# Performance work log

Measured on AMD Instinct MI355X. Metric: run time of the kernel, lower is better.

## Reference

```python
import jax, jax.numpy as jnp
import numpy as np
from jax import lax

K = 20        # cfgs.k: knn size for edge-conv graph features
OUT_K = 8     # cfgs.out_k: knn size for output aggregation
OUT_DIM = 256
EPS = 1e-5    # BatchNorm eps (torch default), training-mode batch stats


def _bn(y, g, b, axes):
    m = y.mean(axes, keepdims=True)
    v = y.var(axes, keepdims=True)  # biased var, as torch BN uses for normalization
    return (y - m) * lax.rsqrt(v + EPS) * g + b


def _graph_feature(x, k):
    # x: [B,N,C] -> [B,N,k,2C] = concat(neighbor - center, center)
    xx = jnp.sum(x * x, axis=-1)                          # [B,N]
    inner = jnp.einsum('bnc,bmc->bnm', x, x)              # [B,N,N]
    neg_d = 2.0 * inner - xx[:, :, None] - xx[:, None, :]  # -||xi-xj||^2
    idx = lax.top_k(neg_d, k)[1]                          # [B,N,k] nearest (incl. self)
    nbr = jax.vmap(lambda p, i: p[i])(x, idx)             # [B,N,k,C]
    ctr = jnp.broadcast_to(x[:, :, None, :], nbr.shape)
    return jnp.concatenate([nbr - ctr, ctr], axis=-1)


def _edgeconv(x, w, g, b):
    # x: [B,N,C] -> [B,N,O]; conv2d 1x1 (no bias) + BN + LeakyReLU(0.2) + max over k
    f = _graph_feature(x, K)                              # [B,N,K,2C]
    y = jnp.einsum('bnkc,oc->bnko', f, w)
    y = jax.nn.leaky_relu(_bn(y, g, b, (0, 1, 2)), 0.2)
    return y.max(axis=2)


def _fps(pts, npoint):
    # furthest point sampling, start at index 0 (pointnet2 convention). pts: [B,N,3]
    B, N, _ = pts.shape
    d0 = jnp.full((B, N), 1e10, pts.dtype)
    first = jnp.zeros((B,), jnp.int32)

    def step(carry, _):
        dist, last = carry
        lp = jnp.take_along_axis(pts, last[:, None, None], axis=1)  # [B,1,3]
        d = jnp.sum((pts - lp) ** 2, axis=-1)
        dist = jnp.minimum(dist, d)
        nxt = jnp.argmax(dist, axis=-1).astype(jnp.int32)
        return (dist, nxt), nxt

    _, rest = lax.scan(step, (d0, first), None, length=npoint - 1)
    return jnp.concatenate([first[:, None], rest.T], axis=1)  # [B,npoint]


def reference(x, w1, g1, b1, w2, g2, b2, wf, gf, bf, wc, gc, bc):
    B, N, _ = x.shape
    # edge-conv block 1: 6 -> 64
    x1 = _edgeconv(x, w1, g1, b1)                         # [B,N,64]
    n1 = N // 2
    _ = _fps(x, n1)  # points[1]; unused when f_layer == c_layer == 2
    # edge-conv block 2: 128 -> 64
    x2 = _edgeconv(x1, w2, g2, b2)                        # [B,N,64]
    n2 = n1 // 2
    idx2 = _fps(x, n2)                                    # [B,M]
    p2 = jax.vmap(lambda p, i: p[i])(x, idx2)             # [B,M,3]
    # KNN(support=x points, query=p2): indices of OUT_K nearest support points
    d = jnp.sum((p2[:, :, None, :] - x[:, None, :, :]) ** 2, axis=-1)  # [B,M,N]
    knn_idx = lax.top_k(-d, OUT_K)[1]                     # [B,M,OUT_K]
    # gather neighbor features from x2 and mean over neighbors
    agg = jax.vmap(lambda f, i: f[i])(x2, knn_idx).mean(axis=2)        # [B,M,64]
    f_out = _bn(jnp.einsum('bmc,oc->bmo', agg, wf), gf, bf, (0, 1)).transpose(0, 2, 1)
    c_out = _bn(jnp.einsum('bmc,oc->bmo', agg, wc), gc, bc, (0, 1)).transpose(0, 2, 1)
    mask = jnp.ones((B, n2), dtype=bool)
    return (f_out, c_out, p2, p2, mask, mask)


def setup_inputs() -> dict:
    key = jax.random.key(0)
    ks = jax.random.split(key, 6)
    B, N = 4, 4096
    x = jax.random.normal(ks[0], (B, N, 3), jnp.float32)
    def w(k, o, c):
        return jax.random.normal(k, (o, c), jnp.float32) / np.sqrt(c)
    return {
        'x': x,
        'w1': w(ks[1], 64, 6),   'g1': jnp.ones(64),  'b1': jnp.zeros(64),
        'w2': w(ks[2], 64, 128), 'g2': jnp.ones(64),  'b2': jnp.zeros(64),
        'wf': w(ks[3], OUT_DIM, 64), 'gf': jnp.ones(OUT_DIM), 'bf': jnp.zeros(OUT_DIM),
        'wc': w(ks[4], OUT_DIM, 64), 'gc': jnp.ones(OUT_DIM), 'bc': jnp.zeros(OUT_DIM),
    }
```

## Files before the change

### kernel.cpp

```cpp
#include <hip/hip_runtime.h>

#define WB 4
#define WN 4096
#define WKNN 20
#define WM 1024
#define WOUTK 8
#define WOD 256
#define BEPS 1e-5f

typedef unsigned long long u64;
typedef unsigned int u32;

#define ACC_F    0
#define IDX1_I   2048
#define IDX2NN_I 329728
#define IDX2_I   657408
#define X1_F     661504
#define XX1_F    1710080
#define X2_F     1726464

#define O_F   0
#define O_C   1048576
#define O_P2A 2097152
#define O_P2B 2109440
#define O_M0  2121728
#define O_M1  2125824

__device__ __forceinline__ u64 shflx64(u64 v, int m){
    int lo = __shfl_xor((int)(u32)(v & 0xFFFFFFFFull), m, 64);
    int hi = __shfl_xor((int)(u32)(v >> 32), m, 64);
    return ((u64)(u32)hi << 32) | (u32)lo;
}
__device__ __forceinline__ u32 encf(float d){
    u32 u = __float_as_uint(d);
    return (u & 0x80000000u) ? ~u : (u | 0x80000000u);
}
template<int L>
__device__ __forceinline__ void ins(u64* lst, u64 key){
    if (key < lst[L-1]){
        #pragma unroll
        for (int j = 0; j < L; ++j){
            u64 a = lst[j];
            u64 mn = key < a ? key : a;
            u64 mx = key < a ? a : key;
            lst[j] = mn; key = mx;
        }
    }
}

template<int CTRL, int RM>
__device__ __forceinline__ void dppsel(double& k, float& x, float& y, float& z){
    int lo = __double2loint(k), hi = __double2hiint(k);
    int slo = __builtin_amdgcn_update_dpp(lo, lo, CTRL, RM, 0xF, false);
    int shi = __builtin_amdgcn_update_dpp(hi, hi, CTRL, RM, 0xF, false);
    int sx = __builtin_amdgcn_update_dpp(__float_as_int(x), __float_as_int(x), CTRL, RM, 0xF, false);
    int sy = __builtin_amdgcn_update_dpp(__float_as_int(y), __float_as_int(y), CTRL, RM, 0xF, false);
    int sz = __builtin_amdgcn_update_dpp(__float_as_int(z), __float_as_int(z), CTRL, RM, 0xF, false);
    double ok = __hiloint2double(shi, slo);
    bool t = ok > k;
    k = t ? ok : k;
    x = t ? __int_as_float(sx) : x;
    y = t ? __int_as_float(sy) : y;
    z = t ? __int_as_float(sz) : z;
}

__global__ __launch_bounds__(512,1)
void k1_fps_knn1(const float* __restrict__ x, float* __restrict__ out,
                 int* __restrict__ idx1, int* __restrict__ idx2){
    __shared__ float px[WN], py[WN], pz[WN];
    __shared__ double wk[2][4];
    __shared__ float wx4[2][4], wy4[2][4], wz4[2][4];
    int tid = threadIdx.x;
    if (blockIdx.x < 4){
        int b = (int)blockIdx.x;
        const float* xb = x + b*WN*3;
        if (tid >= 256){
            for (int i = tid-256; i < WM; i += 256){
                out[O_M0 + b*WM + i] = 1.0f;
                out[O_M1 + b*WM + i] = 1.0f;
            }
            for (int it=1; it<WM; ++it) __syncthreads();
        } else {
            float ptx[16],pty[16],ptz[16],dst[16];
            #pragma unroll
            for (int j=0;j<16;++j){
                int p = tid + j*256;
                ptx[j]=xb[p*3]; pty[j]=xb[p*3+1]; ptz[j]=xb[p*3+2];
                dst[j]=1e10f;
            }
            float lx=xb[0], ly=xb[1], lz=xb[2];
            if (tid==0){
                idx2[b*WM] = 0;
                int o3 = (b*WM)*3;
                out[O_P2A+o3]=lx; out[O_P2A+o3+1]=ly; out[O_P2A+o3+2]=lz;
                out[O_P2B+o3]=lx; out[O_P2B+o3+1]=ly; out[O_P2B+o3+2]=lz;
            }
            int w = tid>>6, lane = tid&63;
            for (int it=1; it<WM; ++it){
                double bk = -1.0; float bx=lx, by=ly, bz=lz;
                #pragma unroll
                for (int j=0;j<16;++j){
                    float dx=ptx[j]-lx, dy=pty[j]-ly, dz=ptz[j]-lz;
                    float d = dx*dx + dy*dy + dz*dz;
                    d = fminf(dst[j], d); dst[j] = d;
                    double kd = __hiloint2double(__float_as_int(d),
                                                 4095 - (tid + j*256));
                    bool t = kd > bk;
                    bk = t?kd:bk; bx = t?ptx[j]:bx; by = t?pty[j]:by; bz = t?ptz[j]:bz;
                }
                dppsel<0x111,0xF>(bk,bx,by,bz);
                dppsel<0x112,0xF>(bk,bx,by,bz);
                dppsel<0x114,0xF>(bk,bx,by,bz);
                dppsel<0x118,0xF>(bk,bx,by,bz);
                dppsel<0x142,0xA>(bk,bx,by,bz);
                dppsel<0x143,0xC>(bk,bx,by,bz);
                int ib = it & 1;
                if (lane==63){ wk[ib][w]=bk; wx4[ib][w]=bx; wy4[ib][w]=by; wz4[ib][w]=bz; }
                __syncthreads();
                int e = lane & 3;
                double gk = wk[ib][e];
                float gx = wx4[ib][e], gy = wy4[ib][e], gz = wz4[ib][e];
                dppsel<0xB1,0xF>(gk,gx,gy,gz);
                dppsel<0x4E,0xF>(gk,gx,gy,gz);
                lx = gx; ly = gy; lz = gz;
                if (tid==0){
                    int last = 4095 - (int)(u32)__double2loint(gk);
                    idx2[b*WM+it] = last;
                    int o3 = (b*WM+it)*3;
                    out[O_P2A+o3]=lx; out[O_P2A+o3+1]=ly; out[O_P2A+o3+2]=lz;
                    out[O_P2B+o3]=lx; out[O_P2B+o3+1]=ly; out[O_P2B+o3+2]=lz;
                }
            }
        }
    } else {
        int kb = (int)blockIdx.x - 4;
        int b = kb >> 9;
        const float* xb = x + b*WN*3;
        for (int i = tid; i < WN*3; i += 512){
            float v = xb[i];
            int n = i/3, c = i - n*3;
            if (c==0) px[n]=v; else if (c==1) py[n]=v; else pz[n]=v;
        }
        __syncthreads();
        int wid = tid>>6, lane = tid&63;
        int n = (kb & 511)*8 + wid;
        int grow = b*WN + n;
        float qx=px[n], qy=py[n], qz=pz[n];
        float qq = qx*qx+qy*qy+qz*qz;
        u64 lst[WKNN];
        #pragma unroll
        for (int j=0;j<WKNN;++j) lst[j]=~0ull;
        for (int t=0;t<64;++t){
            int c = lane + t*64;
            float sx=px[c], sy=py[c], sz=pz[c];
            float ss = sx*sx+sy*sy+sz*sz;
            float inner = qx*sx+qy*sy+qz*sz;
            float nd = (2.0f*inner - qq) - ss;
            u64 key = ((u64)(0xFFFFFFFFu - encf(nd))<<32) | (u32)c;
            ins<WKNN>(lst, key);
        }
        int ob = grow*WKNN;
        for (int r=0;r<WKNN;++r){
            u64 k = lst[0];
            #pragma unroll
            for (int m=32;m;m>>=1){ u64 o = shflx64(k,m); k = o<k?o:k; }
            if (lane==0) idx1[ob+r] = (int)(k & 0xFFFFFFFFu);
            if (lst[0]==k){
                #pragma unroll
                for (int j=0;j<WKNN-1;++j) lst[j]=lst[j+1];
                lst[WKNN-1]=~0ull;
            }
        }
    }
}

__global__ __launch_bounds__(256,1)
void k2_ec1_stats(const float* __restrict__ x, const float* __restrict__ w1,
                  const int* __restrict__ idx1, float* __restrict__ acc){
    __shared__ float as[64], aq[64];
    int tid = threadIdx.x;
    if (tid < 64){ as[tid]=0.f; aq[tid]=0.f; }
    __syncthreads();
    int cg = tid & 7, sg = tid >> 3;
    int chb = cg*8;
    float w[8][6];
    #pragma unroll
    for (int i=0;i<8;++i){
        #pragma unroll
        for (int j=0;j<6;++j) w[i][j] = w1[(chb+i)*6+j];
    }
    float s[8]={0,0,0,0,0,0,0,0}, q[8]={0,0,0,0,0,0,0,0};
    int s0 = (int)blockIdx.x*1024 + sg*32;
    for (int i=0;i<32;++i){
        int smp = s0+i;
        int bn = smp/WKNN;
        int j = idx1[smp];
        int bb = bn >> 12;
        const float* ct = x + bn*3;
        const float* nb = x + (bb*WN + j)*3;
        float c0=ct[0],c1=ct[1],c2=ct[2];
        float f0=nb[0]-c0, f1=nb[1]-c1, f2=nb[2]-c2;
        #pragma unroll
        for (int c=0;c<8;++c){
            float y = w[c][0]*f0 + w[c][1]*f1 + w[c][2]*f2
                    + w[c][3]*c0 + w[c][4]*c1 + w[c][5]*c2;
            s[c] += y; q[c] = fmaf(y,y,q[c]);
        }
    }
    #pragma unroll
    for (int c=0;c<8;++c){ atomicAdd(&as[chb+c], s[c]); atomicAdd(&aq[chb+c], q[c]); }
    __syncthreads();
    if (tid < 64){ atomicAdd(&acc[tid], as[tid]); atomicAdd(&acc[64+tid], aq[tid]); }
}

__global__ __launch_bounds__(256,1)
void k4_ec1_apply(const float* __restrict__ x, const float* __restrict__ w1,
                  const float* __restrict__ g1, const float* __restrict__ b1,
                  const int* __restrict__ idx1, const float* __restrict__ acc,
                  float* __restrict__ x1){
    int lin = (int)blockIdx.x*256 + threadIdx.x;
    int row = lin >> 3, cg = lin & 7, chb = cg*8;
    int bb = row >> 12;
    const float Pinv = 1.0f/(float)(WB*WN*WKNN);
    float aa[8], cc[8], w[8][6];
    #pragma unroll
    for (int i=0;i<8;++i){
        int ch = chb+i;
        float mean = acc[ch]*Pinv;
        float var  = acc[64+ch]*Pinv - mean*mean;
        float rstd = rsqrtf(var + BEPS);
        aa[i] = g1[ch]*rstd;
        cc[i] = b1[ch] - mean*aa[i];
        #pragma unroll
        for (int j=0;j<6;++j) w[i][j]=w1[ch*6+j];
    }
    const float* ct = x + row*3;
    float c0=ct[0],c1=ct[1],c2=ct[2];
    float mx[8];
    #pragma unroll
    for (int i=0;i<8;++i) mx[i] = -1e30f;
    for (int k=0;k<WKNN;++k){
        int j = idx1[row*WKNN+k];
        const float* nb = x + (bb*WN + j)*3;
        float f0=nb[0]-c0, f1=nb[1]-c1, f2=nb[2]-c2;
        #pragma unroll
        for (int c=0;c<8;++c){
            float y = w[c][0]*f0 + w[c][1]*f1 + w[c][2]*f2
                    + w[c][3]*c0 + w[c][4]*c1 + w[c][5]*c2;
            float v = fmaf(y, aa[c], cc[c]);
            v = fmaxf(v, 0.2f*v);
            mx[c] = fmaxf(mx[c], v);
        }
    }
    #pragma unroll
    for (int c=0;c<8;++c) x1[row*64 + chb + c] = mx[c];
}

__global__ __launch_bounds__(256,1)
void k5_xx1(const float* __restrict__ x1, float* __restrict__ xx1){
    int wid = threadIdx.x>>6, lane = threadIdx.x&63;
    int row = (int)blockIdx.x*4 + wid;
    float v = x1[row*64+lane];
    float s = v*v;
    #pragma unroll
    for (int m=32;m;m>>=1) s += __shfl_xor(s,m,64);
    if (lane==0) xx1[row]=s;
}

__global__ __launch_bounds__(512,1)
void k6_knn2(const float* __restrict__ x1, const float* __restrict__ xx1,
             int* __restrict__ idx2nn){
    __shared__ __align__(16) float Qt[64*64];
    __shared__ __align__(16) float St[128*68];
    __shared__ float Sxx[128];
    float* Dt = St;
    int tid = threadIdx.x, wid = tid>>6, lane = tid&63;
    int b = (int)blockIdx.x >> 6, qt = (int)blockIdx.x & 63;
    const float* xb = x1 + b*WN*64;
    for (int i=tid; i<64*16; i+=512){
        int r = i>>4, c4 = i&15;
        *(float4*)&Qt[r*64 + c4*4] = *(const float4*)&xb[(qt*64+r)*64 + c4*4];
    }
    float qxx[8];
    #pragma unroll
    for (int i=0;i<8;++i) qxx[i] = xx1[b*WN + qt*64 + wid*8 + i];
    u64 lst[WKNN];
    #pragma unroll
    for (int j=0;j<WKNN;++j) lst[j]=~0ull;
    int sq = tid>>3, seg = tid&7;
    for (int ct=0; ct<32; ++ct){
        int cb = ct*128;
        __syncthreads();
        for (int i=tid; i<128*16; i+=512){
            int r=i>>4, c4=i&15;
            *(float4*)&St[r*68 + c4*4] = *(const float4*)&xb[(cb+r)*64 + c4*4];
        }
        if (tid < 128) Sxx[tid] = xx1[b*WN + cb + tid];
        __syncthreads();
        float acc[8][2];
        #pragma unroll
        for (int i=0;i<8;++i){ acc[i][0]=0.f; acc[i][1]=0.f; }
        #pragma unroll 4
        for (int d4=0; d4<16; ++d4){
            float4 s0 = *(const float4*)&St[lane*68 + d4*4];
            float4 s1 = *(const float4*)&St[(lane+64)*68 + d4*4];
            #pragma unroll
            for (int i=0;i<8;++i){
                float4 qv = *(const float4*)&Qt[(wid*8+i)*64 + d4*4];
                acc[i][0] += qv.x*s0.x + qv.y*s0.y + qv.z*s0.z + qv.w*s0.w;
                acc[i][1] += qv.x*s1.x + qv.y*s1.y + qv.z*s1.z + qv.w*s1.w;
            }
        }
        __syncthreads();
        float sx0 = Sxx[lane], sx1 = Sxx[lane+64];
        #pragma unroll
        for (int i=0;i<8;++i){
            int r = wid*8+i;
            Dt[r*132 + lane]      = (2.0f*acc[i][0] - qxx[i]) - sx0;
            Dt[r*132 + lane + 64] = (2.0f*acc[i][1] - qxx[i]) - sx1;
        }
        __syncthreads();
        #pragma unroll
        for (int m=0;m<16;++m){
            int col = seg*16+m;
            float nd = Dt[sq*132 + col];
            u64 key = ((u64)(0xFFFFFFFFu - encf(nd))<<32) | (u32)(cb+col);
            ins<WKNN>(lst,key);
        }
    }
    int ob = (b*WN + qt*64 + sq)*WKNN;
    for (int r=0;r<WKNN;++r){
        u64 k = lst[0];
        #pragma unroll
        for (int m=4;m;m>>=1){ u64 o=shflx64(k,m); k = o<k?o:k; }
        if ((tid&7)==0) idx2nn[ob+r] = (int)(k & 0xFFFFFFFFu);
        if (lst[0]==k){
            #pragma unroll
            for (int j=0;j<WKNN-1;++j) lst[j]=lst[j+1];
            lst[WKNN-1]=~0ull;
        }
    }
}

__global__ __launch_bounds__(512,1)
void k7_ec2_stats(const float* __restrict__ x1, const float* __restrict__ w2,
                  const int* __restrict__ idx2nn, float* __restrict__ acc){
    __shared__ __align__(16) float wsm[64*128];
    __shared__ float as[64], aq[64];
    int tid = threadIdx.x, wid = tid>>6, lane = tid&63;
    for (int i=tid; i<2048; i+=512)
        *(float4*)&wsm[i*4] = *(const float4*)&w2[i*4];
    if (tid<64){ as[tid]=0.f; aq[tid]=0.f; }
    __syncthreads();
    int row = (int)blockIdx.x*64 + lane;
    int b = row >> 12;
    const float* xr  = x1 + row*64;
    const float* xbb = x1 + b*WN*64;
    float ss[8]={0,0,0,0,0,0,0,0}, qs[8]={0,0,0,0,0,0,0,0};
    for (int kc=0; kc<5; ++kc){
        int jj[4];
        #pragma unroll
        for (int kk=0;kk<4;++kk) jj[kk] = idx2nn[row*WKNN + kc*4 + kk];
        float av[8][4];
        #pragma unroll
        for (int c=0;c<8;++c){ av[c][0]=0;av[c][1]=0;av[c][2]=0;av[c][3]=0; }
        #pragma unroll 4
        for (int dc=0; dc<16; ++dc){
            float4 cv = *(const float4*)&xr[dc*4];
            float4 fv[4];
            #pragma unroll
            for (int kk=0;kk<4;++kk){
                float4 nv = *(const float4*)&xbb[jj[kk]*64 + dc*4];
                fv[kk].x=nv.x-cv.x; fv[kk].y=nv.y-cv.y; fv[kk].z=nv.z-cv.z; fv[kk].w=nv.w-cv.w;
            }
            #pragma unroll
            for (int c=0;c<8;++c){
                float4 wv = *(const float4*)&wsm[(wid*8+c)*128 + dc*4];
                #pragma unroll
                for (int kk=0;kk<4;++kk)
                    av[c][kk] += wv.x*fv[kk].x + wv.y*fv[kk].y + wv.z*fv[kk].z + wv.w*fv[kk].w;
            }
        }
        #pragma unroll 4
        for (int dc=16; dc<32; ++dc){
            float4 cv = *(const float4*)&xr[(dc-16)*4];
            #pragma unroll
            for (int c=0;c<8;++c){
                float4 wv = *(const float4*)&wsm[(wid*8+c)*128 + dc*4];
                float dv = wv.x*cv.x + wv.y*cv.y + wv.z*cv.z + wv.w*cv.w;
                #pragma unroll
                for (int kk=0;kk<4;++kk) av[c][kk] += dv;
            }
        }
        #pragma unroll
        for (int c=0;c<8;++c){
            #pragma unroll
            for (int kk=0;kk<4;++kk){ ss[c]+=av[c][kk]; qs[c]=fmaf(av[c][kk],av[c][kk],qs[c]); }
        }
    }
    #pragma unroll
    for (int c=0;c<8;++c){ atomicAdd(&as[wid*8+c], ss[c]); atomicAdd(&aq[wid*8+c], qs[c]); }
    __syncthreads();
    if (tid<64){ atomicAdd(&acc[128+tid], as[tid]); atomicAdd(&acc[192+tid], aq[tid]); }
}

__global__ __launch_bounds__(512,1)
void k9_ec2_apply(const float* __restrict__ x1, const float* __restrict__ w2,
                  const float* __restrict__ g2, const float* __restrict__ b2,
                  const int* __restrict__ idx2nn, const float* __restrict__ acc,
                  float* __restrict__ x2){
    __shared__ __align__(16) float wsm[64*128];
    int tid = threadIdx.x, wid = tid>>6, lane = tid&63;
    for (int i=tid; i<2048; i+=512)
        *(float4*)&wsm[i*4] = *(const float4*)&w2[i*4];
    __syncthreads();
    const float Pinv = 1.0f/(float)(WB*WN*WKNN);
    float aa[8], cc[8];
    #pragma unroll
    for (int c=0;c<8;++c){
        int ch = wid*8+c;
        float mean = acc[128+ch]*Pinv;
        float var  = acc[192+ch]*Pinv - mean*mean;
        float rstd = rsqrtf(var + BEPS);
        aa[c] = g2[ch]*rstd;
        cc[c] = b2[ch] - mean*aa[c];
    }
    int row = (int)blockIdx.x*64 + lane;
    int b = row>>12;
    const float* xr  = x1 + row*64;
    const float* xbb = x1 + b*WN*64;
    float mx[8];
    #pragma unroll
    for (int c=0;c<8;++c) mx[c] = -1e30f;
    for (int kc=0;kc<5;++kc){
        int jj[4];
        #pragma unroll
        for (int kk=0;kk<4;++kk) jj[kk]=idx2nn[row*WKNN+kc*4+kk];
        float av[8][4];
        #pragma unroll
        for (int c=0;c<8;++c){ av[c][0]=0;av[c][1]=0;av[c][2]=0;av[c][3]=0; }
        #pragma unroll 4
        for (int dc=0;dc<16;++dc){
            float4 cv = *(const float4*)&xr[dc*4];
            float4 fv[4];
            #pragma unroll
            for (int kk=0;kk<4;++kk){
                float4 nv = *(const float4*)&xbb[jj[kk]*64 + dc*4];
                fv[kk].x=nv.x-cv.x; fv[kk].y=nv.y-cv.y; fv[kk].z=nv.z-cv.z; fv[kk].w=nv.w-cv.w;
            }
            #pragma unroll
            for (int c=0;c<8;++c){
                float4 wv = *(const float4*)&wsm[(wid*8+c)*128 + dc*4];
                #pragma unroll
                for (int kk=0;kk<4;++kk)
                    av[c][kk] += wv.x*fv[kk].x + wv.y*fv[kk].y + wv.z*fv[kk].z + wv.w*fv[kk].w;
            }
        }
        #pragma unroll 4
        for (int dc=16;dc<32;++dc){
            float4 cv = *(const float4*)&xr[(dc-16)*4];
            #pragma unroll
            for (int c=0;c<8;++c){
                float4 wv = *(const float4*)&wsm[(wid*8+c)*128 + dc*4];
                float dv = wv.x*cv.x + wv.y*cv.y + wv.z*cv.z + wv.w*cv.w;
                #pragma unroll
                for (int kk=0;kk<4;++kk) av[c][kk] += dv;
            }
        }
        #pragma unroll
        for (int c=0;c<8;++c){
            #pragma unroll
            for (int kk=0;kk<4;++kk){
                float v = fmaf(av[c][kk], aa[c], cc[c]);
                v = fmaxf(v, 0.2f*v);
                mx[c] = fmaxf(mx[c], v);
            }
        }
    }
    #pragma unroll
    for (int c=0;c<8;++c) x2[row*64 + wid*8 + c] = mx[c];
}

__global__ __launch_bounds__(256,1)
void k10_out(const float* __restrict__ x, const float* __restrict__ x2,
             const int* __restrict__ idx2, const float* __restrict__ wf,
             const float* __restrict__ wc, float* __restrict__ out,
             float* __restrict__ acc){
    __shared__ float px[WN], py[WN], pz[WN];
    __shared__ __align__(16) float aggs[4][64];
    __shared__ float sacc[1024];
    int tid=threadIdx.x, wid=tid>>6, lane=tid&63;
    int b = (int)blockIdx.x >> 6;
    int mb = ((int)blockIdx.x & 63)*16;
    const float* xb = x + b*WN*3;
    for (int i=tid;i<WN*3;i+=256){
        float v=xb[i]; int n=i/3,c=i-n*3;
        if(c==0)px[n]=v; else if(c==1)py[n]=v; else pz[n]=v;
    }
    for (int i=tid;i<1024;i+=256) sacc[i]=0.f;
    __syncthreads();
    for (int qq=0;qq<4;++qq){
        int m = mb + wid*4 + qq;
        int pi = idx2[b*WM+m];
        float qx=px[pi], qy=py[pi], qz=pz[pi];
        u64 lst[WOUTK];
        #pragma unroll
        for (int j=0;j<WOUTK;++j) lst[j]=~0ull;
        for (int t=0;t<64;++t){
            int c = lane + t*64;
            float dx=qx-px[c], dy=qy-py[c], dz=qz-pz[c];
            float d = dx*dx+dy*dy+dz*dz;
            u64 key = ((u64)encf(d)<<32) | (u32)c;
            ins<WOUTK>(lst,key);
        }
        int jr[WOUTK];
        #pragma unroll
        for (int r=0;r<WOUTK;++r){
            u64 k=lst[0];
            #pragma unroll
            for (int mm=32;mm;mm>>=1){ u64 o=shflx64(k,mm); k = o<k?o:k; }
            jr[r] = (int)(k&0xFFFFFFFFu);
            if (lst[0]==k){
                #pragma unroll
                for (int j=0;j<WOUTK-1;++j) lst[j]=lst[j+1];
                lst[WOUTK-1]=~0ull;
            }
        }
        float a = 0.f;
        #pragma unroll
        for (int r=0;r<WOUTK;++r) a += x2[(b*WN + jr[r])*64 + lane];
        a *= 0.125f;
        aggs[wid][lane] = a;
        __syncthreads();
        #pragma unroll
        for (int i=0;i<4;++i){
            int o = lane + 64*i;
            const float4* wfp = (const float4*)(wf + o*64);
            const float4* wcp = (const float4*)(wc + o*64);
            float af=0.f, ac=0.f;
            #pragma unroll
            for (int d4=0;d4<16;++d4){
                float4 avv = *(const float4*)&aggs[wid][d4*4];
                float4 w1v = wfp[d4];
                float4 w2v = wcp[d4];
                af += w1v.x*avv.x + w1v.y*avv.y + w1v.z*avv.z + w1v.w*avv.w;
                ac += w2v.x*avv.x + w2v.y*avv.y + w2v.z*avv.z + w2v.w*avv.w;
            }
            out[O_F + (b*WOD + o)*WM + m] = af;
            out[O_C + (b*WOD + o)*WM + m] = ac;
            atomicAdd(&sacc[o],       af);
            atomicAdd(&sacc[256+o],   af*af);
            atomicAdd(&sacc[512+o],   ac);
            atomicAdd(&sacc[768+o],   ac*ac);
        }
        __syncthreads();
    }
    for (int i=tid;i<1024;i+=256) atomicAdd(&acc[256+i], sacc[i]);
}

__global__ __launch_bounds__(256,1)
void k12_final(const float* __restrict__ acc,
               const float* __restrict__ gf, const float* __restrict__ bf,
               const float* __restrict__ gc, const float* __restrict__ bc,
               float* __restrict__ out){
    int t = (int)blockIdx.x*256 + threadIdx.x;
    int half = t >> 20;
    int r = t & 0xFFFFF;
    int o = (r >> 10) & 255;
    const float Pinv = 1.0f/4096.0f;
    float sum = acc[(half?768:256) + o];
    float sq  = acc[(half?1024:512) + o];
    float mean = sum*Pinv;
    float var  = sq*Pinv - mean*mean;
    float rstd = rsqrtf(var + BEPS);
    float g  = half ? gc[o] : gf[o];
    float bb = half ? bc[o] : bf[o];
    float y = out[t];
    out[t] = (y-mean)*rstd*g + bb;
}

extern "C" void kernel_launch(void* const* d_in, const int* in_sizes, int n_in,
                              void* d_out, int out_size, void* d_ws, size_t ws_size,
                              hipStream_t stream){
    const float* x  = (const float*)d_in[0];
    const float* w1 = (const float*)d_in[1];
    const float* g1 = (const float*)d_in[2];
    const float* b1 = (const float*)d_in[3];
    const float* w2 = (const float*)d_in[4];
    const float* g2 = (const float*)d_in[5];
    const float* b2 = (const float*)d_in[6];
    const float* wf = (const float*)d_in[7];
    const float* gf = (const float*)d_in[8];
    const float* bf = (const float*)d_in[9];
    const float* wc = (const float*)d_in[10];
    const float* gc = (const float*)d_in[11];
    const float* bc = (const float*)d_in[12];
    float* out = (float*)d_out;
    float* wsf = (float*)d_ws;
    int*   wsi = (int*)d_ws;
    float* ACC    = wsf + ACC_F;
    int*   idx1   = wsi + IDX1_I;
    int*   idx2nn = wsi + IDX2NN_I;
    int*   idx2   = wsi + IDX2_I;
    float* x1     = wsf + X1_F;
    float* xx1    = wsf + XX1_F;
    float* x2     = wsf + X2_F;

    hipMemsetAsync(ACC, 0, 1280*sizeof(float), stream);
    k1_fps_knn1 <<<2052,512,0,stream>>>(x,out,idx1,idx2);
    k2_ec1_stats<<<320, 256, 0,stream>>>(x,w1,idx1,ACC);
    k4_ec1_apply<<<512, 256, 0,stream>>>(x,w1,g1,b1,idx1,ACC,x1);
    k5_xx1      <<<4096,256, 0,stream>>>(x1,xx1);
    k6_knn2     <<<256, 512, 0,stream>>>(x1,xx1,idx2nn);
    k7_ec2_stats<<<256, 512, 0,stream>>>(x1,w2,idx2nn,ACC);
    k9_ec2_apply<<<256, 512, 0,stream>>>(x1,w2,g2,b2,idx2nn,ACC,x2);
    k10_out     <<<256, 256, 0,stream>>>(x,x2,idx2,wf,wc,out,ACC);
    k12_final   <<<8192,256, 0,stream>>>(ACC,gf,bf,gc,bc,out);
}
```

Measured before the change: 2.004 ms.

## Fuse all stages into one persistent kernel with software grid barriers

Replaces the chain of nine kernel launches with a single persistent kernel. Four blocks run FPS concurrently while 256 worker blocks step through knn1, the edge-conv stats and apply, knn2, the output stage and the final BN, separated by atomic-counter grid barriers. The FPS blocks now use all 512 threads with 8 points each and an 8-wave reduction, and FPS is overlapped with the rest of the pipeline through a flag. This removes launch gaps and lets the serial FPS hide behind other work, at the cost of relying on all 260 blocks being co-resident and on spin barriers that have timeout escapes.

```diff
diff --git a/kernel.cpp b/kernel.cpp
--- a/kernel.cpp
+++ b/kernel.cpp
@@ -12,6 +12,8 @@
 typedef unsigned int u32;
 
 #define ACC_F    0
+#define CTR_WBAR 1280
+#define CTR_FPS  1281
 #define IDX1_I   2048
 #define IDX2NN_I 329728
 #define IDX2_I   657408
@@ -64,107 +66,314 @@
     z = t ? __int_as_float(sz) : z;
 }
 
+struct SmemA { float px[WN], py[WN], pz[WN]; double wk[2][8]; float wx[2][8], wy[2][8], wz[2][8]; };
+struct SmemB { float Qt[64*64]; float St[128*68]; float Sxx[128]; };
+struct SmemC { float wsm[64*128]; float as[64], aq[64]; };
+struct SmemD { float px[WN], py[WN], pz[WN]; float aggs[8][64]; float sacc[1024]; };
+union Smem { SmemA a; SmemB b; SmemC c; SmemD d; };
+
+__device__ __forceinline__ void wbar(u32* ctr, u32 target){
+    __syncthreads();
+    if (threadIdx.x == 0){
+        __threadfence();
+        __hip_atomic_fetch_add(ctr, 1u, __ATOMIC_ACQ_REL, __HIP_MEMORY_SCOPE_AGENT);
+        long long spins = 0;
+        while (__hip_atomic_load(ctr, __ATOMIC_ACQUIRE, __HIP_MEMORY_SCOPE_AGENT) < target){
+            __builtin_amdgcn_s_sleep(8);
+            if (++spins > (1LL<<22)) break;
+        }
+        __threadfence();
+    }
+    __syncthreads();
+}
+__device__ __forceinline__ void wait_flag(u32* ctr, u32 target){
+    __syncthreads();
+    if (threadIdx.x == 0){
+        long long spins = 0;
+        while (__hip_atomic_load(ctr, __ATOMIC_ACQUIRE, __HIP_MEMORY_SCOPE_AGENT) < target){
+            __builtin_amdgcn_s_sleep(8);
+            if (++spins > (1LL<<22)) break;
+        }
+        __threadfence();
+    }
+    __syncthreads();
+}
+
 __global__ __launch_bounds__(512,1)
-void k1_fps_knn1(const float* __restrict__ x, float* __restrict__ out,
-                 int* __restrict__ idx1, int* __restrict__ idx2){
-    __shared__ float px[WN], py[WN], pz[WN];
-    __shared__ double wk[2][4];
-    __shared__ float wx4[2][4], wy4[2][4], wz4[2][4];
+void mega(const float* __restrict__ x,
+          const float* __restrict__ w1, const float* __restrict__ g1, const float* __restrict__ b1,
+          const float* __restrict__ w2, const float* __restrict__ g2, const float* __restrict__ b2,
+          const float* __restrict__ wf, const float* __restrict__ gf, const float* __restrict__ bf,
+          const float* __restrict__ wc, const float* __restrict__ gc, const float* __restrict__ bc,
+          float* __restrict__ out, float* __restrict__ wsf, int* __restrict__ wsi)
+{
+    __shared__ Smem sm;
+    float* acc    = wsf + ACC_F;
+    int*   idx1   = wsi + IDX1_I;
+    int*   idx2nn = wsi + IDX2NN_I;
+    int*   idx2   = wsi + IDX2_I;
+    float* x1     = wsf + X1_F;
+    float* xx1    = wsf + XX1_F;
+    float* x2     = wsf + X2_F;
+    u32* wctr = (u32*)(wsi + CTR_WBAR);
+    u32* fctr = (u32*)(wsi + CTR_FPS);
     int tid = threadIdx.x;
+
     if (blockIdx.x < 4){
         int b = (int)blockIdx.x;
         const float* xb = x + b*WN*3;
-        if (tid >= 256){
-            for (int i = tid-256; i < WM; i += 256){
-                out[O_M0 + b*WM + i] = 1.0f;
-                out[O_M1 + b*WM + i] = 1.0f;
-            }
-            for (int it=1; it<WM; ++it) __syncthreads();
-        } else {
-            float ptx[16],pty[16],ptz[16],dst[16];
-            #pragma unroll
-            for (int j=0;j<16;++j){
-                int p = tid + j*256;
-                ptx[j]=xb[p*3]; pty[j]=xb[p*3+1]; ptz[j]=xb[p*3+2];
-                dst[j]=1e10f;
-            }
-            float lx=xb[0], ly=xb[1], lz=xb[2];
+        for (int i = tid; i < WM; i += 512){
+            out[O_M0 + b*WM + i] = 1.0f;
+            out[O_M1 + b*WM + i] = 1.0f;
+        }
+        float ptx[8],pty[8],ptz[8],dst[8];
+        #pragma unroll
+        for (int j=0;j<8;++j){
+            int p = tid + j*512;
+            ptx[j]=xb[p*3]; pty[j]=xb[p*3+1]; ptz[j]=xb[p*3+2];
+            dst[j]=1e10f;
+        }
+        float lx=xb[0], ly=xb[1], lz=xb[2];
+        if (tid==0){
+            idx2[b*WM] = 0;
+            int o3 = (b*WM)*3;
+            out[O_P2A+o3]=lx; out[O_P2A+o3+1]=ly; out[O_P2A+o3+2]=lz;
+            out[O_P2B+o3]=lx; out[O_P2B+o3+1]=ly; out[O_P2B+o3+2]=lz;
+        }
+        int w = tid>>6, lane = tid&63;
+        int base = 4095 - tid;
+        for (int it=1; it<WM; ++it){
+            double bk = -1.0; float bx=lx, by=ly, bz=lz;
+            #pragma unroll
+            for (int j=0;j<8;++j){
+                float dx=ptx[j]-lx, dy=pty[j]-ly, dz=ptz[j]-lz;
+                float d = dx*dx + dy*dy + dz*dz;
+                d = fminf(dst[j], d); dst[j] = d;
+                double kd = __hiloint2double(__float_as_int(d), base - j*512);
+                bool t = kd > bk;
+                bk = t?kd:bk; bx = t?ptx[j]:bx; by = t?pty[j]:by; bz = t?ptz[j]:bz;
+            }
+            dppsel<0x111,0xF>(bk,bx,by,bz);
+            dppsel<0x112,0xF>(bk,bx,by,bz);
+            dppsel<0x114,0xF>(bk,bx,by,bz);
+            dppsel<0x118,0xF>(bk,bx,by,bz);
+            dppsel<0x142,0xA>(bk,bx,by,bz);
+            dppsel<0x143,0xC>(bk,bx,by,bz);
+            int ib = it & 1;
+            if (lane==63){ sm.a.wk[ib][w]=bk; sm.a.wx[ib][w]=bx; sm.a.wy[ib][w]=by; sm.a.wz[ib][w]=bz; }
+            __syncthreads();
+            int e = lane & 3;
+            double k0 = sm.a.wk[ib][e],   k1 = sm.a.wk[ib][e+4];
+            float x0 = sm.a.wx[ib][e],   y0 = sm.a.wy[ib][e],   z0 = sm.a.wz[ib][e];
+            float x1v= sm.a.wx[ib][e+4], y1v= sm.a.wy[ib][e+4], z1v= sm.a.wz[ib][e+4];
+            bool t8 = k1 > k0;
+            double gk = t8?k1:k0;
+            float gx = t8?x1v:x0, gy = t8?y1v:y0, gz = t8?z1v:z0;
+            dppsel<0xB1,0xF>(gk,gx,gy,gz);
+            dppsel<0x4E,0xF>(gk,gx,gy,gz);
+            lx = gx; ly = gy; lz = gz;
             if (tid==0){
-                idx2[b*WM] = 0;
-                int o3 = (b*WM)*3;
+                int last = 4095 - (int)(u32)__double2loint(gk);
+                idx2[b*WM+it] = last;
+                int o3 = (b*WM+it)*3;
                 out[O_P2A+o3]=lx; out[O_P2A+o3+1]=ly; out[O_P2A+o3+2]=lz;
                 out[O_P2B+o3]=lx; out[O_P2B+o3+1]=ly; out[O_P2B+o3+2]=lz;
             }
-            int w = tid>>6, lane = tid&63;
-            for (int it=1; it<WM; ++it){
-                double bk = -1.0; float bx=lx, by=ly, bz=lz;
-                #pragma unroll
-                for (int j=0;j<16;++j){
-                    float dx=ptx[j]-lx, dy=pty[j]-ly, dz=ptz[j]-lz;
-                    float d = dx*dx + dy*dy + dz*dz;
-                    d = fminf(dst[j], d); dst[j] = d;
-                    double kd = __hiloint2double(__float_as_int(d),
-                                                 4095 - (tid + j*256));
-                    bool t = kd > bk;
-                    bk = t?kd:bk; bx = t?ptx[j]:bx; by = t?pty[j]:by; bz = t?ptz[j]:bz;
-                }
-                dppsel<0x111,0xF>(bk,bx,by,bz);
-                dppsel<0x112,0xF>(bk,bx,by,bz);
-                dppsel<0x114,0xF>(bk,bx,by,bz);
-                dppsel<0x118,0xF>(bk,bx,by,bz);
-                dppsel<0x142,0xA>(bk,bx,by,bz);
-                dppsel<0x143,0xC>(bk,bx,by,bz);
-                int ib = it & 1;
-                if (lane==63){ wk[ib][w]=bk; wx4[ib][w]=bx; wy4[ib][w]=by; wz4[ib][w]=bz; }
-                __syncthreads();
-                int e = lane & 3;
-                double gk = wk[ib][e];
-                float gx = wx4[ib][e], gy = wy4[ib][e], gz = wz4[ib][e];
-                dppsel<0xB1,0xF>(gk,gx,gy,gz);
-                dppsel<0x4E,0xF>(gk,gx,gy,gz);
-                lx = gx; ly = gy; lz = gz;
-                if (tid==0){
-                    int last = 4095 - (int)(u32)__double2loint(gk);
-                    idx2[b*WM+it] = last;
-                    int o3 = (b*WM+it)*3;
-                    out[O_P2A+o3]=lx; out[O_P2A+o3+1]=ly; out[O_P2A+o3+2]=lz;
-                    out[O_P2B+o3]=lx; out[O_P2B+o3+1]=ly; out[O_P2B+o3+2]=lz;
-                }
-            }
-        }
-    } else {
-        int kb = (int)blockIdx.x - 4;
-        int b = kb >> 9;
-        const float* xb = x + b*WN*3;
+        }
+        __syncthreads();
+        if (tid==0){
+            __threadfence();
+            __hip_atomic_fetch_add(fctr, 1u, __ATOMIC_RELEASE, __HIP_MEMORY_SCOPE_AGENT);
+        }
+        return;
+    }
+
+    int wb = (int)blockIdx.x - 4;
+    int wid = tid>>6, lane = tid&63;
+
+    {
+        int bb = wb >> 6;
+        const float* xbk = x + bb*WN*3;
         for (int i = tid; i < WN*3; i += 512){
-            float v = xb[i];
+            float v = xbk[i];
             int n = i/3, c = i - n*3;
-            if (c==0) px[n]=v; else if (c==1) py[n]=v; else pz[n]=v;
-        }
-        __syncthreads();
-        int wid = tid>>6, lane = tid&63;
-        int n = (kb & 511)*8 + wid;
-        int grow = b*WN + n;
-        float qx=px[n], qy=py[n], qz=pz[n];
-        float qq = qx*qx+qy*qy+qz*qz;
+            if (c==0) sm.a.px[n]=v; else if (c==1) sm.a.py[n]=v; else sm.a.pz[n]=v;
+        }
+        __syncthreads();
+        for (int rr=0; rr<8; ++rr){
+            int n = (wb&63)*64 + wid*8 + rr;
+            float qx=sm.a.px[n], qy=sm.a.py[n], qz=sm.a.pz[n];
+            float qq = qx*qx+qy*qy+qz*qz;
+            u64 lst[WKNN];
+            #pragma unroll
+            for (int j=0;j<WKNN;++j) lst[j]=~0ull;
+            for (int t=0;t<64;++t){
+                int c = lane + t*64;
+                float sx=sm.a.px[c], sy=sm.a.py[c], sz=sm.a.pz[c];
+                float ss = sx*sx+sy*sy+sz*sz;
+                float inner = qx*sx+qy*sy+qz*sz;
+                float nd = (2.0f*inner - qq) - ss;
+                u64 key = ((u64)(0xFFFFFFFFu - encf(nd))<<32) | (u32)c;
+                ins<WKNN>(lst, key);
+            }
+            int ob = (bb*WN + n)*WKNN;
+            for (int r=0;r<WKNN;++r){
+                u64 k = lst[0];
+                #pragma unroll
+                for (int m=32;m;m>>=1){ u64 o = shflx64(k,m); k = o<k?o:k; }
+                if (lane==0) idx1[ob+r] = (int)(k & 0xFFFFFFFFu);
+                if (lst[0]==k){
+                    #pragma unroll
+                    for (int j=0;j<WKNN-1;++j) lst[j]=lst[j+1];
+                    lst[WKNN-1]=~0ull;
+                }
+            }
+        }
+    }
+    wbar(wctr, 256*1);
+
+    {
+        if (tid < 64){ sm.c.as[tid]=0.f; sm.c.aq[tid]=0.f; }
+        __syncthreads();
+        int cg = tid & 7, sg = tid >> 3, chb = cg*8;
+        float w[8][6];
+        #pragma unroll
+        for (int i=0;i<8;++i){
+            #pragma unroll
+            for (int j=0;j<6;++j) w[i][j] = w1[(chb+i)*6+j];
+        }
+        float s[8]={0,0,0,0,0,0,0,0}, q[8]={0,0,0,0,0,0,0,0};
+        int s0 = wb*1280 + sg*20;
+        for (int i=0;i<20;++i){
+            int smp = s0+i;
+            int bn = smp/WKNN;
+            int j = idx1[smp];
+            int bb2 = bn >> 12;
+            const float* ct = x + bn*3;
+            const float* nb = x + (bb2*WN + j)*3;
+            float c0=ct[0],c1=ct[1],c2=ct[2];
+            float f0=nb[0]-c0, f1=nb[1]-c1, f2=nb[2]-c2;
+            #pragma unroll
+            for (int c=0;c<8;++c){
+                float y = w[c][0]*f0 + w[c][1]*f1 + w[c][2]*f2
+                        + w[c][3]*c0 + w[c][4]*c1 + w[c][5]*c2;
+                s[c] += y; q[c] = fmaf(y,y,q[c]);
+            }
+        }
+        #pragma unroll
+        for (int c=0;c<8;++c){ atomicAdd(&sm.c.as[chb+c], s[c]); atomicAdd(&sm.c.aq[chb+c], q[c]); }
+        __syncthreads();
+        if (tid < 64){ atomicAdd(&acc[tid], sm.c.as[tid]); atomicAdd(&acc[64+tid], sm.c.aq[tid]); }
+    }
+    wbar(wctr, 256*2);
+
+    {
+        int lin = wb*512 + tid;
+        int row = lin >> 3, cg = lin & 7, chb = cg*8;
+        int bb2 = row >> 12;
+        const float Pinv = 1.0f/(float)(WB*WN*WKNN);
+        float aa[8], cc[8], w[8][6];
+        #pragma unroll
+        for (int i=0;i<8;++i){
+            int ch = chb+i;
+            float mean = acc[ch]*Pinv;
+            float var  = acc[64+ch]*Pinv - mean*mean;
+            float rstd = rsqrtf(var + BEPS);
+            aa[i] = g1[ch]*rstd;
+            cc[i] = b1[ch] - mean*aa[i];
+            #pragma unroll
+            for (int j=0;j<6;++j) w[i][j]=w1[ch*6+j];
+        }
+        const float* ct = x + row*3;
+        float c0=ct[0],c1=ct[1],c2=ct[2];
+        float mx[8];
+        #pragma unroll
+        for (int i=0;i<8;++i) mx[i] = -1e30f;
+        for (int k=0;k<WKNN;++k){
+            int j = idx1[row*WKNN+k];
+            const float* nb = x + (bb2*WN + j)*3;
+            float f0=nb[0]-c0, f1=nb[1]-c1, f2=nb[2]-c2;
+            #pragma unroll
+            for (int c=0;c<8;++c){
+                float y = w[c][0]*f0 + w[c][1]*f1 + w[c][2]*f2
+                        + w[c][3]*c0 + w[c][4]*c1 + w[c][5]*c2;
+                float v = fmaf(y, aa[c], cc[c]);
+                v = fmaxf(v, 0.2f*v);
+                mx[c] = fmaxf(mx[c], v);
+            }
+        }
+        float sq2 = 0.f;
+        #pragma unroll
+        for (int c=0;c<8;++c){ x1[row*64 + chb + c] = mx[c]; sq2 = fmaf(mx[c],mx[c],sq2); }
+        sq2 += __shfl_xor(sq2,1,64);
+        sq2 += __shfl_xor(sq2,2,64);
+        sq2 += __shfl_xor(sq2,4,64);
+        if ((tid&7)==0) xx1[row] = sq2;
+    }
+    wbar(wctr, 256*3);
+
+    {
+        float* Qt = sm.b.Qt; float* St = sm.b.St; float* Sxx = sm.b.Sxx;
+        float* Dt = St;
+        int b2 = wb >> 6, qt = wb & 63;
+        const float* xbf = x1 + b2*WN*64;
+        for (int i=tid; i<64*16; i+=512){
+            int r = i>>4, c4 = i&15;
+            *(float4*)&Qt[r*64 + c4*4] = *(const float4*)&xbf[(qt*64+r)*64 + c4*4];
+        }
+        float qxx[8];
+        #pragma unroll
+        for (int i=0;i<8;++i) qxx[i] = xx1[b2*WN + qt*64 + wid*8 + i];
         u64 lst[WKNN];
         #pragma unroll
         for (int j=0;j<WKNN;++j) lst[j]=~0ull;
-        for (int t=0;t<64;++t){
-            int c = lane + t*64;
-            float sx=px[c], sy=py[c], sz=pz[c];
-            float ss = sx*sx+sy*sy+sz*sz;
-            float inner = qx*sx+qy*sy+qz*sz;
-            float nd = (2.0f*inner - qq) - ss;
-            u64 key = ((u64)(0xFFFFFFFFu - encf(nd))<<32) | (u32)c;
-            ins<WKNN>(lst, key);
-        }
-        int ob = grow*WKNN;
+        int sq = tid>>3, seg = tid&7;
+        for (int ct=0; ct<32; ++ct){
+            int cb = ct*128;
+            __syncthreads();
+            for (int i=tid; i<128*16; i+=512){
+                int r=i>>4, c4=i&15;
+                *(float4*)&St[r*68 + c4*4] = *(const float4*)&xbf[(cb+r)*64 + c4*4];
+            }
+            if (tid < 128) Sxx[tid] = xx1[b2*WN + cb + tid];
+            __syncthreads();
+            float a2[8][2];
+            #pragma unroll
+            for (int i=0;i<8;++i){ a2[i][0]=0.f; a2[i][1]=0.f; }
+            #pragma unroll 4
+            for (int d4=0; d4<16; ++d4){
+                float4 s0 = *(const float4*)&St[lane*68 + d4*4];
+                float4 s1 = *(const float4*)&St[(lane+64)*68 + d4*4];
+                #pragma unroll
+                for (int i=0;i<8;++i){
+                    float4 qv = *(const float4*)&Qt[(wid*8+i)*64 + d4*4];
+                    a2[i][0] += qv.x*s0.x + qv.y*s0.y + qv.z*s0.z + qv.w*s0.w;
+                    a2[i][1] += qv.x*s1.x + qv.y*s1.y + qv.z*s1.z + qv.w*s1.w;
+                }
+            }
+            __syncthreads();
+            float sx0 = Sxx[lane], sx1 = Sxx[lane+64];
+            #pragma unroll
+            for (int i=0;i<8;++i){
+                int r = wid*8+i;
+                Dt[r*132 + lane]      = (2.0f*a2[i][0] - qxx[i]) - sx0;
+                Dt[r*132 + lane + 64] = (2.0f*a2[i][1] - qxx[i]) - sx1;
+            }
+            __syncthreads();
+            #pragma unroll
+            for (int m=0;m<16;++m){
+                int col = seg*16+m;
+                float nd = Dt[sq*132 + col];
+                u64 key = ((u64)(0xFFFFFFFFu - encf(nd))<<32) | (u32)(cb+col);
+                ins<WKNN>(lst,key);
+            }
+        }
+        int ob = (b2*WN + qt*64 + sq)*WKNN;
         for (int r=0;r<WKNN;++r){
             u64 k = lst[0];
             #pragma unroll
-            for (int m=32;m;m>>=1){ u64 o = shflx64(k,m); k = o<k?o:k; }
-            if (lane==0) idx1[ob+r] = (int)(k & 0xFFFFFFFFu);
+            for (int m=4;m;m>>=1){ u64 o=shflx64(k,m); k = o<k?o:k; }
+            if ((tid&7)==0) idx2nn[ob+r] = (int)(k & 0xFFFFFFFFu);
             if (lst[0]==k){
                 #pragma unroll
                 for (int j=0;j<WKNN-1;++j) lst[j]=lst[j+1];
@@ -172,411 +381,230 @@
             }
         }
     }
-}
-
-__global__ __launch_bounds__(256,1)
-void k2_ec1_stats(const float* __restrict__ x, const float* __restrict__ w1,
-                  const int* __restrict__ idx1, float* __restrict__ acc){
-    __shared__ float as[64], aq[64];
-    int tid = threadIdx.x;
-    if (tid < 64){ as[tid]=0.f; aq[tid]=0.f; }
-    __syncthreads();
-    int cg = tid & 7, sg = tid >> 3;
-    int chb = cg*8;
-    float w[8][6];
-    #pragma unroll
-    for (int i=0;i<8;++i){
-        #pragma unroll
-        for (int j=0;j<6;++j) w[i][j] = w1[(chb+i)*6+j];
-    }
-    float s[8]={0,0,0,0,0,0,0,0}, q[8]={0,0,0,0,0,0,0,0};
-    int s0 = (int)blockIdx.x*1024 + sg*32;
-    for (int i=0;i<32;++i){
-        int smp = s0+i;
-        int bn = smp/WKNN;
-        int j = idx1[smp];
-        int bb = bn >> 12;
-        const float* ct = x + bn*3;
-        const float* nb = x + (bb*WN + j)*3;
-        float c0=ct[0],c1=ct[1],c2=ct[2];
-        float f0=nb[0]-c0, f1=nb[1]-c1, f2=nb[2]-c2;
+    wbar(wctr, 256*4);
+
+    {
+        float* wsm = sm.c.wsm;
+        for (int i=tid; i<2048; i+=512)
+            *(float4*)&wsm[i*4] = *(const float4*)&w2[i*4];
+        if (tid<64){ sm.c.as[tid]=0.f; sm.c.aq[tid]=0.f; }
+        __syncthreads();
+        int row = wb*64 + lane;
+        int b2 = row >> 12;
+        const float* xr  = x1 + row*64;
+        const float* xbb = x1 + b2*WN*64;
+        float ss[8]={0,0,0,0,0,0,0,0}, qs[8]={0,0,0,0,0,0,0,0};
+        for (int kc=0; kc<5; ++kc){
+            int jj[4];
+            #pragma unroll
+            for (int kk=0;kk<4;++kk) jj[kk] = idx2nn[row*WKNN + kc*4 + kk];
+            float av[8][4];
+            #pragma unroll
+            for (int c=0;c<8;++c){ av[c][0]=0;av[c][1]=0;av[c][2]=0;av[c][3]=0; }
+            #pragma unroll 4
+            for (int dc=0; dc<16; ++dc){
+                float4 cv = *(const float4*)&xr[dc*4];
+                float4 fv[4];
+                #pragma unroll
+                for (int kk=0;kk<4;++kk){
+                    float4 nv = *(const float4*)&xbb[jj[kk]*64 + dc*4];
+                    fv[kk].x=nv.x-cv.x; fv[kk].y=nv.y-cv.y; fv[kk].z=nv.z-cv.z; fv[kk].w=nv.w-cv.w;
+                }
+                #pragma unroll
+                for (int c=0;c<8;++c){
+                    float4 wv = *(const float4*)&wsm[(wid*8+c)*128 + dc*4];
+                    #pragma unroll
+                    for (int kk=0;kk<4;++kk)
+                        av[c][kk] += wv.x*fv[kk].x + wv.y*fv[kk].y + wv.z*fv[kk].z + wv.w*fv[kk].w;
+                }
+            }
+            #pragma unroll 4
+            for (int dc=16; dc<32; ++dc){
+                float4 cv = *(const float4*)&xr[(dc-16)*4];
+                #pragma unroll
+                for (int c=0;c<8;++c){
+                    float4 wv = *(const float4*)&wsm[(wid*8+c)*128 + dc*4];
+                    float dv = wv.x*cv.x + wv.y*cv.y + wv.z*cv.z + wv.w*cv.w;
+                    #pragma unroll
+                    for (int kk=0;kk<4;++kk) av[c][kk] += dv;
+                }
+            }
+            #pragma unroll
+            for (int c=0;c<8;++c){
+                #pragma unroll
+                for (int kk=0;kk<4;++kk){ ss[c]+=av[c][kk]; qs[c]=fmaf(av[c][kk],av[c][kk],qs[c]); }
+            }
+        }
+        #pragma unroll
+        for (int c=0;c<8;++c){ atomicAdd(&sm.c.as[wid*8+c], ss[c]); atomicAdd(&sm.c.aq[wid*8+c], qs[c]); }
+        __syncthreads();
+        if (tid<64){ atomicAdd(&acc[128+tid], sm.c.as[tid]); atomicAdd(&acc[192+tid], sm.c.aq[tid]); }
+    }
+    wbar(wctr, 256*5);
+
+    {
+        float* wsm = sm.c.wsm;
+        for (int i=tid; i<2048; i+=512)
+            *(float4*)&wsm[i*4] = *(const float4*)&w2[i*4];
+        __syncthreads();
+        const float Pinv = 1.0f/(float)(WB*WN*WKNN);
+        float aa[8], cc[8];
         #pragma unroll
         for (int c=0;c<8;++c){
-            float y = w[c][0]*f0 + w[c][1]*f1 + w[c][2]*f2
-                    + w[c][3]*c0 + w[c][4]*c1 + w[c][5]*c2;
-            s[c] += y; q[c] = fmaf(y,y,q[c]);
-        }
-    }
-    #pragma unroll
-    for (int c=0;c<8;++c){ atomicAdd(&as[chb+c], s[c]); atomicAdd(&aq[chb+c], q[c]); }
-    __syncthreads();
-    if (tid < 64){ atomicAdd(&acc[tid], as[tid]); atomicAdd(&acc[64+tid], aq[tid]); }
-}
-
-__global__ __launch_bounds__(256,1)
-void k4_ec1_apply(const float* __restrict__ x, const float* __restrict__ w1,
-                  const float* __restrict__ g1, const float* __restrict__ b1,
-                  const int* __restrict__ idx1, const float* __restrict__ acc,
-                  float* __restrict__ x1){
-    int lin = (int)blockIdx.x*256 + threadIdx.x;
-    int row = lin >> 3, cg = lin & 7, chb = cg*8;
-    int bb = row >> 12;
-    const float Pinv = 1.0f/(float)(WB*WN*WKNN);
-    float aa[8], cc[8], w[8][6];
-    #pragma unroll
-    for (int i=0;i<8;++i){
-        int ch = chb+i;
-        float mean = acc[ch]*Pinv;
-        float var  = acc[64+ch]*Pinv - mean*mean;
-        float rstd = rsqrtf(var + BEPS);
-        aa[i] = g1[ch]*rstd;
-        cc[i] = b1[ch] - mean*aa[i];
-        #pragma unroll
-        for (int j=0;j<6;++j) w[i][j]=w1[ch*6+j];
-    }
-    const float* ct = x + row*3;
-    float c0=ct[0],c1=ct[1],c2=ct[2];
-    float mx[8];
-    #pragma unroll
-    for (int i=0;i<8;++i) mx[i] = -1e30f;
-    for (int k=0;k<WKNN;++k){
-        int j = idx1[row*WKNN+k];
-        const float* nb = x + (bb*WN + j)*3;
-        float f0=nb[0]-c0, f1=nb[1]-c1, f2=nb[2]-c2;
-        #pragma unroll
-        for (int c=0;c<8;++c){
-            float y = w[c][0]*f0 + w[c][1]*f1 + w[c][2]*f2
-                    + w[c][3]*c0 + w[c][4]*c1 + w[c][5]*c2;
-            float v = fmaf(y, aa[c], cc[c]);
-            v = fmaxf(v, 0.2f*v);
-            mx[c] = fmaxf(mx[c], v);
-        }
-    }
-    #pragma unroll
-    for (int c=0;c<8;++c) x1[row*64 + chb + c] = mx[c];
-}
-
-__global__ __launch_bounds__(256,1)
-void k5_xx1(const float* __restrict__ x1, float* __restrict__ xx1){
-    int wid = threadIdx.x>>6, lane = threadIdx.x&63;
-    int row = (int)blockIdx.x*4 + wid;
-    float v = x1[row*64+lane];
-    float s = v*v;
-    #pragma unroll
-    for (int m=32;m;m>>=1) s += __shfl_xor(s,m,64);
-    if (lane==0) xx1[row]=s;
-}
-
-__global__ __launch_bounds__(512,1)
-void k6_knn2(const float* __restrict__ x1, const float* __restrict__ xx1,
-             int* __restrict__ idx2nn){
-    __shared__ __align__(16) float Qt[64*64];
-    __shared__ __align__(16) float St[128*68];
-    __shared__ float Sxx[128];
-    float* Dt = St;
-    int tid = threadIdx.x, wid = tid>>6, lane = tid&63;
-    int b = (int)blockIdx.x >> 6, qt = (int)blockIdx.x & 63;
-    const float* xb = x1 + b*WN*64;
-    for (int i=tid; i<64*16; i+=512){
-        int r = i>>4, c4 = i&15;
-        *(float4*)&Qt[r*64 + c4*4] = *(const float4*)&xb[(qt*64+r)*64 + c4*4];
-    }
-    float qxx[8];
-    #pragma unroll
-    for (int i=0;i<8;++i) qxx[i] = xx1[b*WN + qt*64 + wid*8 + i];
-    u64 lst[WKNN];
-    #pragma unroll
-    for (int j=0;j<WKNN;++j) lst[j]=~0ull;
-    int sq = tid>>3, seg = tid&7;
-    for (int ct=0; ct<32; ++ct){
-        int cb = ct*128;
-        __syncthreads();
-        for (int i=tid; i<128*16; i+=512){
-            int r=i>>4, c4=i&15;
-            *(float4*)&St[r*68 + c4*4] = *(const float4*)&xb[(cb+r)*64 + c4*4];
-        }
-        if (tid < 128) Sxx[tid] = xx1[b*WN + cb + tid];
-        __syncthreads();
-        float acc[8][2];
-        #pragma unroll
-        for (int i=0;i<8;++i){ acc[i][0]=0.f; acc[i][1]=0.f; }
-        #pragma unroll 4
-        for (int d4=0; d4<16; ++d4){
-            float4 s0 = *(const float4*)&St[lane*68 + d4*4];
-            float4 s1 = *(const float4*)&St[(lane+64)*68 + d4*4];
-            #pragma unroll
-            for (int i=0;i<8;++i){
-                float4 qv = *(const float4*)&Qt[(wid*8+i)*64 + d4*4];
-                acc[i][0] += qv.x*s0.x + qv.y*s0.y + qv.z*s0.z + qv.w*s0.w;
-                acc[i][1] += qv.x*s1.x + qv.y*s1.y + qv.z*s1.z + qv.w*s1.w;
-            }
-        }
-        __syncthreads();
-        float sx0 = Sxx[lane], sx1 = Sxx[lane+64];
-        #pragma unroll
-        for (int i=0;i<8;++i){
-            int r = wid*8+i;
-            Dt[r*132 + lane]      = (2.0f*acc[i][0] - qxx[i]) - sx0;
-            Dt[r*132 + lane + 64] = (2.0f*acc[i][1] - qxx[i]) - sx1;
-        }
-        __syncthreads();
-        #pragma unroll
-        for (int m=0;m<16;++m){
-            int col = seg*16+m;
-            float nd = Dt[sq*132 + col];
-            u64 key = ((u64)(0xFFFFFFFFu - encf(nd))<<32) | (u32)(cb+col);
-            ins<WKNN>(lst,key);
-        }
-    }
-    int ob = (b*WN + qt*64 + sq)*WKNN;
-    for (int r=0;r<WKNN;++r){
-        u64 k = lst[0];
-        #pragma unroll
-        for (int m=4;m;m>>=1){ u64 o=shflx64(k,m); k = o<k?o:k; }
-        if ((tid&7)==0) idx2nn[ob+r] = (int)(k & 0xFFFFFFFFu);
-        if (lst[0]==k){
-            #pragma unroll
-            for (int j=0;j<WKNN-1;++j) lst[j]=lst[j+1];
-            lst[WKNN-1]=~0ull;
-        }
-    }
-}
-
-__global__ __launch_bounds__(512,1)
-void k7_ec2_stats(const float* __restrict__ x1, const float* __restrict__ w2,
-                  const int* __restrict__ idx2nn, float* __restrict__ acc){
-    __shared__ __align__(16) float wsm[64*128];
-    __shared__ float as[64], aq[64];
-    int tid = threadIdx.x, wid = tid>>6, lane = tid&63;
-    for (int i=tid; i<2048; i+=512)
-        *(float4*)&wsm[i*4] = *(const float4*)&w2[i*4];
-    if (tid<64){ as[tid]=0.f; aq[tid]=0.f; }
-    __syncthreads();
-    int row = (int)blockIdx.x*64 + lane;
-    int b = row >> 12;
-    const float* xr  = x1 + row*64;
-    const float* xbb = x1 + b*WN*64;
-    float ss[8]={0,0,0,0,0,0,0,0}, qs[8]={0,0,0,0,0,0,0,0};
-    for (int kc=0; kc<5; ++kc){
-        int jj[4];
-        #pragma unroll
-        for (int kk=0;kk<4;++kk) jj[kk] = idx2nn[row*WKNN + kc*4 + kk];
-        float av[8][4];
-        #pragma unroll
-        for (int c=0;c<8;++c){ av[c][0]=0;av[c][1]=0;av[c][2]=0;av[c][3]=0; }
-        #pragma unroll 4
-        for (int dc=0; dc<16; ++dc){
-            float4 cv = *(const float4*)&xr[dc*4];
-            float4 fv[4];
-            #pragma unroll
-            for (int kk=0;kk<4;++kk){
-                float4 nv = *(const float4*)&xbb[jj[kk]*64 + dc*4];
-                fv[kk].x=nv.x-cv.x; fv[kk].y=nv.y-cv.y; fv[kk].z=nv.z-cv.z; fv[kk].w=nv.w-cv.w;
+            int ch = wid*8+c;
+            float mean = acc[128+ch]*Pinv;
+            float var  = acc[192+ch]*Pinv - mean*mean;
+            float rstd = rsqrtf(var + BEPS);
+            aa[c] = g2[ch]*rstd;
+            cc[c] = b2[ch] - mean*aa[c];
+        }
+        int row = wb*64 + lane;
+        int b2 = row>>12;
+        const float* xr  = x1 + row*64;
+        const float* xbb = x1 + b2*WN*64;
+        float mx[8];
+        #pragma unroll
+        for (int c=0;c<8;++c) mx[c] = -1e30f;
+        for (int kc=0;kc<5;++kc){
+            int jj[4];
+            #pragma unroll
+            for (int kk=0;kk<4;++kk) jj[kk]=idx2nn[row*WKNN+kc*4+kk];
+            float av[8][4];
+            #pragma unroll
+            for (int c=0;c<8;++c){ av[c][0]=0;av[c][1]=0;av[c][2]=0;av[c][3]=0; }
+            #pragma unroll 4
+            for (int dc=0;dc<16;++dc){
+                float4 cv = *(const float4*)&xr[dc*4];
+                float4 fv[4];
+                #pragma unroll
+                for (int kk=0;kk<4;++kk){
+                    float4 nv = *(const float4*)&xbb[jj[kk]*64 + dc*4];
+                    fv[kk].x=nv.x-cv.x; fv[kk].y=nv.y-cv.y; fv[kk].z=nv.z-cv.z; fv[kk].w=nv.w-cv.w;
+                }
+                #pragma unroll
+                for (int c=0;c<8;++c){
+                    float4 wv = *(const float4*)&wsm[(wid*8+c)*128 + dc*4];
+                    #pragma unroll
+                    for (int kk=0;kk<4;++kk)
+                        av[c][kk] += wv.x*fv[kk].x + wv.y*fv[kk].y + wv.z*fv[kk].z + wv.w*fv[kk].w;
+                }
+            }
+            #pragma unroll 4
+            for (int dc=16;dc<32;++dc){
+                float4 cv = *(const float4*)&xr[(dc-16)*4];
+                #pragma unroll
+                for (int c=0;c<8;++c){
+                    float4 wv = *(const float4*)&wsm[(wid*8+c)*128 + dc*4];
+                    float dv = wv.x*cv.x + wv.y*cv.y + wv.z*cv.z + wv.w*cv.w;
+                    #pragma unroll
+                    for (int kk=0;kk<4;++kk) av[c][kk] += dv;
+                }
             }
             #pragma unroll
             for (int c=0;c<8;++c){
-                float4 wv = *(const float4*)&wsm[(wid*8+c)*128 + dc*4];
-                #pragma unroll
-                for (int kk=0;kk<4;++kk)
-                    av[c][kk] += wv.x*fv[kk].x + wv.y*fv[kk].y + wv.z*fv[kk].z + wv.w*fv[kk].w;
-            }
-        }
-        #pragma unroll 4
-        for (int dc=16; dc<32; ++dc){
-            float4 cv = *(const float4*)&xr[(dc-16)*4];
-            #pragma unroll
-            for (int c=0;c<8;++c){
-                float4 wv = *(const float4*)&wsm[(wid*8+c)*128 + dc*4];
-                float dv = wv.x*cv.x + wv.y*cv.y + wv.z*cv.z + wv.w*cv.w;
-                #pragma unroll
-                for (int kk=0;kk<4;++kk) av[c][kk] += dv;
-            }
-        }
-        #pragma unroll
-        for (int c=0;c<8;++c){
-            #pragma unroll
-            for (int kk=0;kk<4;++kk){ ss[c]+=av[c][kk]; qs[c]=fmaf(av[c][kk],av[c][kk],qs[c]); }
-        }
-    }
-    #pragma unroll
-    for (int c=0;c<8;++c){ atomicAdd(&as[wid*8+c], ss[c]); atomicAdd(&aq[wid*8+c], qs[c]); }
-    __syncthreads();
-    if (tid<64){ atomicAdd(&acc[128+tid], as[tid]); atomicAdd(&acc[192+tid], aq[tid]); }
-}
-
-__global__ __launch_bounds__(512,1)
-void k9_ec2_apply(const float* __restrict__ x1, const float* __restrict__ w2,
-                  const float* __restrict__ g2, const float* __restrict__ b2,
-                  const int* __restrict__ idx2nn, const float* __restrict__ acc,
-                  float* __restrict__ x2){
-    __shared__ __align__(16) float wsm[64*128];
-    int tid = threadIdx.x, wid = tid>>6, lane = tid&63;
-    for (int i=tid; i<2048; i+=512)
-        *(float4*)&wsm[i*4] = *(const float4*)&w2[i*4];
-    __syncthreads();
-    const float Pinv = 1.0f/(float)(WB*WN*WKNN);
-    float aa[8], cc[8];
-    #pragma unroll
-    for (int c=0;c<8;++c){
-        int ch = wid*8+c;
-        float mean = acc[128+ch]*Pinv;
-        float var  = acc[192+ch]*Pinv - mean*mean;
-        float rstd = rsqrtf(var + BEPS);
-        aa[c] = g2[ch]*rstd;
-        cc[c] = b2[ch] - mean*aa[c];
-    }
-    int row = (int)blockIdx.x*64 + lane;
-    int b = row>>12;
-    const float* xr  = x1 + row*64;
-    const float* xbb = x1 + b*WN*64;
-    float mx[8];
-    #pragma unroll
-    for (int c=0;c<8;++c) mx[c] = -1e30f;
-    for (int kc=0;kc<5;++kc){
-        int jj[4];
-        #pragma unroll
-        for (int kk=0;kk<4;++kk) jj[kk]=idx2nn[row*WKNN+kc*4+kk];
-        float av[8][4];
-        #pragma unroll
-        for (int c=0;c<8;++c){ av[c][0]=0;av[c][1]=0;av[c][2]=0;av[c][3]=0; }
-        #pragma unroll 4
-        for (int dc=0;dc<16;++dc){
-            float4 cv = *(const float4*)&xr[dc*4];
-            float4 fv[4];
-            #pragma unroll
-            for (int kk=0;kk<4;++kk){
-                float4 nv = *(const float4*)&xbb[jj[kk]*64 + dc*4];
-                fv[kk].x=nv.x-cv.x; fv[kk].y=nv.y-cv.y; fv[kk].z=nv.z-cv.z; fv[kk].w=nv.w-cv.w;
-            }
-            #pragma unroll
-            for (int c=0;c<8;++c){
-                float4 wv = *(const float4*)&wsm[(wid*8+c)*128 + dc*4];
-                #pragma unroll
-                for (int kk=0;kk<4;++kk)
-                    av[c][kk] += wv.x*fv[kk].x + wv.y*fv[kk].y + wv.z*fv[kk].z + wv.w*fv[kk].w;
-            }
-        }
-        #pragma unroll 4
-        for (int dc=16;dc<32;++dc){
-            float4 cv = *(const float4*)&xr[(dc-16)*4];
-            #pragma unroll
-            for (int c=0;c<8;++c){
-                float4 wv = *(const float4*)&wsm[(wid*8+c)*128 + dc*4];
-                float dv = wv.x*cv.x + wv.y*cv.y + wv.z*cv.z + wv.w*cv.w;
-                #pragma unroll
-                for (int kk=0;kk<4;++kk) av[c][kk] += dv;
-            }
-        }
-        #pragma unroll
-        for (int c=0;c<8;++c){
-            #pragma unroll
-            for (int kk=0;kk<4;++kk){
-                float v = fmaf(av[c][kk], aa[c], cc[c]);
-                v = fmaxf(v, 0.2f*v);
-                mx[c] = fmaxf(mx[c], v);
-            }
-        }
-    }
-    #pragma unroll
-    for (int c=0;c<8;++c) x2[row*64 + wid*8 + c] = mx[c];
-}
-
-__global__ __launch_bounds__(256,1)
-void k10_out(const float* __restrict__ x, const float* __restrict__ x2,
-             const int* __restrict__ idx2, const float* __restrict__ wf,
-             const float* __restrict__ wc, float* __restrict__ out,
-             float* __restrict__ acc){
-    __shared__ float px[WN], py[WN], pz[WN];
-    __shared__ __align__(16) float aggs[4][64];
-    __shared__ float sacc[1024];
-    int tid=threadIdx.x, wid=tid>>6, lane=tid&63;
-    int b = (int)blockIdx.x >> 6;
-    int mb = ((int)blockIdx.x & 63)*16;
-    const float* xb = x + b*WN*3;
-    for (int i=tid;i<WN*3;i+=256){
-        float v=xb[i]; int n=i/3,c=i-n*3;
-        if(c==0)px[n]=v; else if(c==1)py[n]=v; else pz[n]=v;
-    }
-    for (int i=tid;i<1024;i+=256) sacc[i]=0.f;
-    __syncthreads();
-    for (int qq=0;qq<4;++qq){
-        int m = mb + wid*4 + qq;
-        int pi = idx2[b*WM+m];
-        float qx=px[pi], qy=py[pi], qz=pz[pi];
-        u64 lst[WOUTK];
-        #pragma unroll
-        for (int j=0;j<WOUTK;++j) lst[j]=~0ull;
-        for (int t=0;t<64;++t){
-            int c = lane + t*64;
-            float dx=qx-px[c], dy=qy-py[c], dz=qz-pz[c];
-            float d = dx*dx+dy*dy+dz*dz;
-            u64 key = ((u64)encf(d)<<32) | (u32)c;
-            ins<WOUTK>(lst,key);
-        }
-        int jr[WOUTK];
-        #pragma unroll
-        for (int r=0;r<WOUTK;++r){
-            u64 k=lst[0];
-            #pragma unroll
-            for (int mm=32;mm;mm>>=1){ u64 o=shflx64(k,mm); k = o<k?o:k; }
-            jr[r] = (int)(k&0xFFFFFFFFu);
-            if (lst[0]==k){
-                #pragma unroll
-                for (int j=0;j<WOUTK-1;++j) lst[j]=lst[j+1];
-                lst[WOUTK-1]=~0ull;
-            }
-        }
-        float a = 0.f;
-        #pragma unroll
-        for (int r=0;r<WOUTK;++r) a += x2[(b*WN + jr[r])*64 + lane];
-        a *= 0.125f;
-        aggs[wid][lane] = a;
-        __syncthreads();
-        #pragma unroll
-        for (int i=0;i<4;++i){
-            int o = lane + 64*i;
-            const float4* wfp = (const float4*)(wf + o*64);
-            const float4* wcp = (const float4*)(wc + o*64);
-            float af=0.f, ac=0.f;
-            #pragma unroll
-            for (int d4=0;d4<16;++d4){
-                float4 avv = *(const float4*)&aggs[wid][d4*4];
-                float4 w1v = wfp[d4];
-                float4 w2v = wcp[d4];
-                af += w1v.x*avv.x + w1v.y*avv.y + w1v.z*avv.z + w1v.w*avv.w;
-                ac += w2v.x*avv.x + w2v.y*avv.y + w2v.z*avv.z + w2v.w*avv.w;
-            }
-            out[O_F + (b*WOD + o)*WM + m] = af;
-            out[O_C + (b*WOD + o)*WM + m] = ac;
-            atomicAdd(&sacc[o],       af);
-            atomicAdd(&sacc[256+o],   af*af);
-            atomicAdd(&sacc[512+o],   ac);
-            atomicAdd(&sacc[768+o],   ac*ac);
-        }
-        __syncthreads();
-    }
-    for (int i=tid;i<1024;i+=256) atomicAdd(&acc[256+i], sacc[i]);
-}
-
-__global__ __launch_bounds__(256,1)
-void k12_final(const float* __restrict__ acc,
-               const float* __restrict__ gf, const float* __restrict__ bf,
-               const float* __restrict__ gc, const float* __restrict__ bc,
-               float* __restrict__ out){
-    int t = (int)blockIdx.x*256 + threadIdx.x;
-    int half = t >> 20;
-    int r = t & 0xFFFFF;
-    int o = (r >> 10) & 255;
-    const float Pinv = 1.0f/4096.0f;
-    float sum = acc[(half?768:256) + o];
-    float sq  = acc[(half?1024:512) + o];
-    float mean = sum*Pinv;
-    float var  = sq*Pinv - mean*mean;
-    float rstd = rsqrtf(var + BEPS);
-    float g  = half ? gc[o] : gf[o];
-    float bb = half ? bc[o] : bf[o];
-    float y = out[t];
-    out[t] = (y-mean)*rstd*g + bb;
+                #pragma unroll
+                for (int kk=0;kk<4;++kk){
+                    float v = fmaf(av[c][kk], aa[c], cc[c]);
+                    v = fmaxf(v, 0.2f*v);
+                    mx[c] = fmaxf(mx[c], v);
+                }
+            }
+        }
+        #pragma unroll
+        for (int c=0;c<8;++c) x2[row*64 + wid*8 + c] = mx[c];
+    }
+    wbar(wctr, 256*6);
+
+    wait_flag(fctr, 4u);
+
+    {
+        int b2 = wb >> 6;
+        int mb = (wb & 63)*16;
+        const float* xb2 = x + b2*WN*3;
+        for (int i=tid;i<WN*3;i+=512){
+            float v=xb2[i]; int n=i/3,c=i-n*3;
+            if(c==0)sm.d.px[n]=v; else if(c==1)sm.d.py[n]=v; else sm.d.pz[n]=v;
+        }
+        for (int i=tid;i<1024;i+=512) sm.d.sacc[i]=0.f;
+        __syncthreads();
+        for (int qq=0;qq<2;++qq){
+            int m = mb + wid*2 + qq;
+            int pi = idx2[b2*WM+m];
+            float qx=sm.d.px[pi], qy=sm.d.py[pi], qz=sm.d.pz[pi];
+            u64 lst[WOUTK];
+            #pragma unroll
+            for (int j=0;j<WOUTK;++j) lst[j]=~0ull;
+            for (int t=0;t<64;++t){
+                int c = lane + t*64;
+                float dx=qx-sm.d.px[c], dy=qy-sm.d.py[c], dz=qz-sm.d.pz[c];
+                float d = dx*dx+dy*dy+dz*dz;
+                u64 key = ((u64)encf(d)<<32) | (u32)c;
+                ins<WOUTK>(lst,key);
+            }
+            int jr[WOUTK];
+            #pragma unroll
+            for (int r=0;r<WOUTK;++r){
+                u64 k=lst[0];
+                #pragma unroll
+                for (int mm=32;mm;mm>>=1){ u64 o=shflx64(k,mm); k = o<k?o:k; }
+                jr[r] = (int)(k&0xFFFFFFFFu);
+                if (lst[0]==k){
+                    #pragma unroll
+                    for (int j=0;j<WOUTK-1;++j) lst[j]=lst[j+1];
+                    lst[WOUTK-1]=~0ull;
+                }
+            }
+            float a = 0.f;
+            #pragma unroll
+            for (int r=0;r<WOUTK;++r) a += x2[(b2*WN + jr[r])*64 + lane];
+            a *= 0.125f;
+            sm.d.aggs[wid][lane] = a;
+            #pragma unroll
+            for (int i2=0;i2<4;++i2){
+                int o = lane + 64*i2;
+                const float4* wfp = (const float4*)(wf + o*64);
+                const float4* wcp = (const float4*)(wc + o*64);
+                float af=0.f, ac=0.f;
+                #pragma unroll
+                for (int d4=0;d4<16;++d4){
+                    float4 avv = *(const float4*)&sm.d.aggs[wid][d4*4];
+                    float4 w1v = wfp[d4];
+                    float4 w2v = wcp[d4];
+                    af += w1v.x*avv.x + w1v.y*avv.y + w1v.z*avv.z + w1v.w*avv.w;
+                    ac += w2v.x*avv.x + w2v.y*avv.y + w2v.z*avv.z + w2v.w*avv.w;
+                }
+                out[O_F + (b2*WOD + o)*WM + m] = af;
+                out[O_C + (b2*WOD + o)*WM + m] = ac;
+                atomicAdd(&sm.d.sacc[o],       af);
+                atomicAdd(&sm.d.sacc[256+o],   af*af);
+                atomicAdd(&sm.d.sacc[512+o],   ac);
+                atomicAdd(&sm.d.sacc[768+o],   ac*ac);
+            }
+        }
+        __syncthreads();
+        for (int i=tid;i<1024;i+=512) atomicAdd(&acc[256+i], sm.d.sacc[i]);
+    }
+    wbar(wctr, 256*7);
+
+    {
+        const float Pinv = 1.0f/4096.0f;
+        int t0 = wb*8192;
+        for (int k=0;k<16;++k){
+            int t = t0 + k*512 + tid;
+            int half = t >> 20;
+            int r = t & 0xFFFFF;
+            int o = (r >> 10) & 255;
+            float sum = acc[(half?768:256) + o];
+            float sq  = acc[(half?1024:512) + o];
+            float mean = sum*Pinv;
+            float var  = sq*Pinv - mean*mean;
+            float rstd = rsqrtf(var + BEPS);
+            float g  = half ? gc[o] : gf[o];
+            float bb = half ? bc[o] : bf[o];
+            float y = out[t];
+            out[t] = (y-mean)*rstd*g + bb;
+        }
+    }
 }
 
 extern "C" void kernel_launch(void* const* d_in, const int* in_sizes, int n_in,
@@ -598,22 +626,7 @@
     float* out = (float*)d_out;
     float* wsf = (float*)d_ws;
     int*   wsi = (int*)d_ws;
-    float* ACC    = wsf + ACC_F;
-    int*   idx1   = wsi + IDX1_I;
-    int*   idx2nn = wsi + IDX2NN_I;
-    int*   idx2   = wsi + IDX2_I;
-    float* x1     = wsf + X1_F;
-    float* xx1    = wsf + XX1_F;
-    float* x2     = wsf + X2_F;
-
-    hipMemsetAsync(ACC, 0, 1280*sizeof(float), stream);
-    k1_fps_knn1 <<<2052,512,0,stream>>>(x,out,idx1,idx2);
-    k2_ec1_stats<<<320, 256, 0,stream>>>(x,w1,idx1,ACC);
-    k4_ec1_apply<<<512, 256, 0,stream>>>(x,w1,g1,b1,idx1,ACC,x1);
-    k5_xx1      <<<4096,256, 0,stream>>>(x1,xx1);
-    k6_knn2     <<<256, 512, 0,stream>>>(x1,xx1,idx2nn);
-    k7_ec2_stats<<<256, 512, 0,stream>>>(x1,w2,idx2nn,ACC);
-    k9_ec2_apply<<<256, 512, 0,stream>>>(x1,w2,g2,b2,idx2nn,ACC,x2);
-    k10_out     <<<256, 256, 0,stream>>>(x,x2,idx2,wf,wc,out,ACC);
-    k12_final   <<<8192,256, 0,stream>>>(ACC,gf,bf,gc,bc,out);
-}
+
+    hipMemsetAsync(wsf, 0, 1288*sizeof(float), stream);
+    mega<<<260,512,0,stream>>>(x,w1,g1,b1,w2,g2,b2,wf,gf,bf,wc,gc,bc,out,wsf,wsi);
+}
```

After: 2.707 ms. +35.1%, slower.
